# Performance work log

Measured on AMD Instinct MI355X. Metric: run time of the kernel, lower is better.

Reference implementation:

```python
import jax, jax.numpy as jnp
import numpy as np

D_MODEL, NHEAD, INT_DIM = 1024, 16, 4096
HEAD_DIM = D_MODEL // NHEAD
EPS = 1e-5


def _layernorm(x, gamma, beta):
    mu = jnp.mean(x, axis=-1, keepdims=True)
    var = jnp.var(x, axis=-1, keepdims=True)
    return (x - mu) * jax.lax.rsqrt(var + EPS) * gamma + beta


def setup_inputs() -> dict:
    key = jax.random.key(0)
    ks = jax.random.split(key, 16)
    B, T = 2, 2048
    s = 0.02
    inp = {
        'x': jax.random.normal(ks[0], (B, T, D_MODEL), dtype=jnp.float32),
        'Wq': jax.random.normal(ks[1], (D_MODEL, D_MODEL), dtype=jnp.float32) * s,
        'bq': jnp.zeros((D_MODEL,), jnp.float32),
        'Wk': jax.random.normal(ks[2], (D_MODEL, D_MODEL), dtype=jnp.float32) * s,
        'bk': jnp.zeros((D_MODEL,), jnp.float32),
        'Wv': jax.random.normal(ks[3], (D_MODEL, D_MODEL), dtype=jnp.float32) * s,
        'bv': jnp.zeros((D_MODEL,), jnp.float32),
        'Wo': jax.random.normal(ks[4], (D_MODEL, D_MODEL), dtype=jnp.float32) * s,
        'bo': jnp.zeros((D_MODEL,), jnp.float32),
        'ln1_g': jnp.ones((D_MODEL,), jnp.float32),
        'ln1_b': jnp.zeros((D_MODEL,), jnp.float32),
        'ln2_g': jnp.ones((D_MODEL,), jnp.float32),
        'ln2_b': jnp.zeros((D_MODEL,), jnp.float32),
        'W1': jax.random.normal(ks[5], (D_MODEL, INT_DIM), dtype=jnp.float32) * s,
        'b1': jnp.zeros((INT_DIM,), jnp.float32),
        'W2': jax.random.normal(ks[6], (INT_DIM, D_MODEL), dtype=jnp.float32) * s,
        'b2': jnp.zeros((D_MODEL,), jnp.float32),
    }
    return inp


def reference(x, Wq, bq, Wk, bk, Wv, bv, Wo, bo, ln1_g, ln1_b, ln2_g, ln2_b, W1, b1, W2, b2):
    B, T, D = x.shape
    # projections
    q = (x @ Wq + bq).reshape(B, T, NHEAD, HEAD_DIM).transpose(0, 2, 1, 3)
    k = (x @ Wk + bk).reshape(B, T, NHEAD, HEAD_DIM).transpose(0, 2, 1, 3)
    v = (x @ Wv + bv).reshape(B, T, NHEAD, HEAD_DIM).transpose(0, 2, 1, 3)
    # attention: [B,H,T,T] scores, softmax over keys
    scores = jnp.einsum('bhqd,bhkd->bhqk', q, k) / jnp.sqrt(jnp.float32(HEAD_DIM))
    attn = jax.nn.softmax(scores, axis=-1)
    out = jnp.einsum('bhqk,bhkd->bhqd', attn, v)
    out = out.transpose(0, 2, 1, 3).reshape(B, T, D)
    attn_output = out @ Wo + bo
    # residual + layernorm 1
    h = _layernorm(x + attn_output, ln1_g, ln1_b)
    # FFN
    ff = jax.nn.relu(h @ W1 + b1) @ W2 + b2
    # residual + layernorm 2
    return _layernorm(h + ff, ln2_g, ln2_b)
```

## Files before the change

kernel.cpp:

```cpp
#include <hip/hip_runtime.h>
#include <cstdint>

#define DEVI __device__ __forceinline__

typedef float f32x4 __attribute__((ext_vector_type(4)));
typedef __bf16 bf16x8 __attribute__((ext_vector_type(8)));
typedef unsigned int u32x4v __attribute__((ext_vector_type(4)));
typedef unsigned short u16;
typedef unsigned int u32;
typedef unsigned long long u64;

#define LOG2E 1.44269504088896f
#define QSCALE (0.125f * LOG2E)

DEVI u16 bf16bits(float f) {
    u32 u = __builtin_bit_cast(u32, f);
    u32 r = u + 0x7fffu + ((u >> 16) & 1u);
    return (u16)(r >> 16);
}

DEVI u32 pack2bf(float a, float b) {
    u16 x = __builtin_bit_cast(u16, (__bf16)a);
    u16 y = __builtin_bit_cast(u16, (__bf16)b);
    return (u32)x | ((u32)y << 16);
}

DEVI void gload16(const void* g, const void* l) {
    __builtin_amdgcn_global_load_lds(
        (const __attribute__((address_space(1))) void*)(u64)(uintptr_t)g,
        (__attribute__((address_space(3))) void*)(u32)(uintptr_t)l,
        16, 0, 0);
}

__global__ __launch_bounds__(256) void cast_bf16_kernel(const float* __restrict__ in,
                                                        u16* __restrict__ out, int n4) {
    int i = blockIdx.x * 256 + threadIdx.x;
    if (i < n4) {
        float4 v = ((const float4*)in)[i];
        u32 lo = bf16bits(v.x) | ((u32)bf16bits(v.y) << 16);
        u32 hi = bf16bits(v.z) | ((u32)bf16bits(v.w) << 16);
        ((uint2*)out)[i] = make_uint2(lo, hi);
    }
}

DEVI void tpose_body(const float* __restrict__ src, u16* __restrict__ dst, int K_, int N_) {
    __shared__ float t[64][65];
    int k0 = blockIdx.x * 64, n0 = blockIdx.y * 64;
    int tid = threadIdx.x;
#pragma unroll
    for (int i = 0; i < 16; i++) {
        int idx = i * 256 + tid;
        int r = idx >> 6, c = idx & 63;
        t[r][c] = src[(u64)(k0 + r) * N_ + n0 + c];
    }
    __syncthreads();
#pragma unroll
    for (int i = 0; i < 16; i++) {
        int idx = i * 256 + tid;
        int r = idx >> 6, c = idx & 63;
        dst[(u64)(n0 + r) * K_ + k0 + c] = bf16bits(t[c][r]);
    }
}

__global__ __launch_bounds__(256) void transpose_cast_kernel(const float* __restrict__ src,
                                                             u16* __restrict__ dst,
                                                             int K_, int N_) {
    tpose_body(src, dst, K_, N_);
}

__global__ __launch_bounds__(256) void transpose_cast4_kernel(
    const float* __restrict__ s0, const float* __restrict__ s1,
    const float* __restrict__ s2, const float* __restrict__ s3,
    u16* __restrict__ d0, u16* __restrict__ d1, u16* __restrict__ d2, u16* __restrict__ d3) {
    int z = blockIdx.z;
    const float* src = z == 0 ? s0 : z == 1 ? s1 : z == 2 ? s2 : s3;
    u16* dst = z == 0 ? d0 : z == 1 ? d1 : z == 2 ? d2 : d3;
    tpose_body(src, dst, 1024, 1024);
}

enum { MODE_QK = 0, MODE_VT = 1, MODE_RESID = 2, MODE_RELU = 3 };

DEVI void gemm_core(const u16* __restrict__ A, const u16* __restrict__ Bt, int K_,
                    u16* ldsA, u16* ldsB, f32x4 (&acc)[4][4], int m0, int n0) {
    const int tid = threadIdx.x;
    const int lane = tid & 63;
    const int wid = tid >> 6;
    const int wr = wid >> 1, wc = wid & 1;
    const int l15 = lane & 15, l4 = lane >> 4;

    for (int kt = 0; kt < K_; kt += 64) {
        __syncthreads();
#pragma unroll
        for (int i = 0; i < 4; i++) {
            int s = i * 256 + tid;
            int row = s >> 3, c = s & 7;
            gload16(A + (u64)(m0 + row) * K_ + kt + ((c ^ (row & 7)) * 8),
                    (const char*)ldsA + s * 16);
        }
#pragma unroll
        for (int i = 0; i < 4; i++) {
            int s = i * 256 + tid;
            int row = s >> 3, c = s & 7;
            gload16(Bt + (u64)(n0 + row) * K_ + kt + ((c ^ (row & 7)) * 8),
                    (const char*)ldsB + s * 16);
        }
        __syncthreads();
#pragma unroll
        for (int ks = 0; ks < 2; ks++) {
            bf16x8 af[4], bfr[4];
#pragma unroll
            for (int mi = 0; mi < 4; mi++) {
                int row = wr * 64 + mi * 16 + l15;
                af[mi] = *(const bf16x8*)((const char*)ldsA + row * 128 +
                                          (((ks * 4 + l4) ^ (row & 7)) * 16));
            }
#pragma unroll
            for (int ni = 0; ni < 4; ni++) {
                int row = wc * 64 + ni * 16 + l15;
                bfr[ni] = *(const bf16x8*)((const char*)ldsB + row * 128 +
                                           (((ks * 4 + l4) ^ (row & 7)) * 16));
            }
            __builtin_amdgcn_s_setprio(1);
#pragma unroll
            for (int mi = 0; mi < 4; mi++)
#pragma unroll
                for (int ni = 0; ni < 4; ni++)
                    acc[mi][ni] = __builtin_amdgcn_mfma_f32_16x16x32_bf16(
                        af[mi], bfr[ni], acc[mi][ni], 0, 0, 0);
            __builtin_amdgcn_s_setprio(0);
        }
    }
}

template <int MODE>
DEVI void gemm_epilogue(f32x4 (&acc)[4][4], const float* __restrict__ bias,
                        const float* __restrict__ resid, void* __restrict__ outp,
                        int N_, int m0, int n0, float scale) {
    const int tid = threadIdx.x;
    const int lane = tid & 63;
    const int wid = tid >> 6;
    const int wr = wid >> 1, wc = wid & 1;
    const int l15 = lane & 15, l4 = lane >> 4;
#pragma unroll
    for (int mi = 0; mi < 4; mi++) {
#pragma unroll
        for (int ni = 0; ni < 4; ni++) {
            const int n = n0 + wc * 64 + ni * 16 + l15;
            const float bv = bias[n];
            const int mb = m0 + wr * 64 + mi * 16 + l4 * 4;
            if (MODE == MODE_VT) {
                const int b = mb >> 11, t = mb & 2047;
                const int hh = n >> 6, d = n & 63;
                u32 lo = pack2bf(acc[mi][ni][0] + bv, acc[mi][ni][1] + bv);
                u32 hi = pack2bf(acc[mi][ni][2] + bv, acc[mi][ni][3] + bv);
                u64 idx = ((u64)((b << 4) + hh) * 64 + d) * 2048 + t;
                *(uint2*)((u16*)outp + idx) = make_uint2(lo, hi);
            } else {
#pragma unroll
                for (int r = 0; r < 4; r++) {
                    const int m = mb + r;
                    const float v = acc[mi][ni][r] + bv;
                    if (MODE == MODE_QK) {
                        const int b = m >> 11, t = m & 2047;
                        const int hh = n >> 6, d = n & 63;
                        ((u16*)outp)[(((u64)((b << 4) + hh) * 2048 + t) << 6) + d] =
                            bf16bits(v * scale);
                    } else if (MODE == MODE_RESID) {
                        const u64 i2 = (u64)m * N_ + n;
                        ((float*)outp)[i2] = v + resid[i2];
                    } else {
                        ((u16*)outp)[(u64)m * N_ + n] = bf16bits(fmaxf(v, 0.f));
                    }
                }
            }
        }
    }
}

template <int MODE>
__global__ __launch_bounds__(256, 2)
void gemm_kernel(const u16* __restrict__ A, const u16* __restrict__ Bt,
                 const float* __restrict__ bias, const float* __restrict__ resid,
                 void* __restrict__ outp, int N_, int K_) {
    __shared__ u16 ldsA[128 * 64];
    __shared__ u16 ldsB[128 * 64];
    const int m0 = blockIdx.x * 128;
    const int n0 = blockIdx.y * 128;
    f32x4 acc[4][4];
#pragma unroll
    for (int i = 0; i < 4; i++)
#pragma unroll
        for (int j = 0; j < 4; j++) acc[i][j] = (f32x4){0.f, 0.f, 0.f, 0.f};
    gemm_core(A, Bt, K_, ldsA, ldsB, acc, m0, n0);
    gemm_epilogue<MODE>(acc, bias, resid, outp, N_, m0, n0, 1.f);
}

__global__ __launch_bounds__(256, 2)
void gemm_qkv_kernel(const u16* __restrict__ A,
                     const u16* __restrict__ Wq, const u16* __restrict__ Wk,
                     const u16* __restrict__ Wv,
                     const float* __restrict__ bq, const float* __restrict__ bk,
                     const float* __restrict__ bv,
                     u16* __restrict__ Qo, u16* __restrict__ Ko, u16* __restrict__ Vo) {
    __shared__ u16 ldsA[128 * 64];
    __shared__ u16 ldsB[128 * 64];
    const int z = blockIdx.z;
    const u16* Bt = z == 0 ? Wq : z == 1 ? Wk : Wv;
    const float* bias = z == 0 ? bq : z == 1 ? bk : bv;
    const int m0 = blockIdx.x * 128;
    const int n0 = blockIdx.y * 128;
    f32x4 acc[4][4];
#pragma unroll
    for (int i = 0; i < 4; i++)
#pragma unroll
        for (int j = 0; j < 4; j++) acc[i][j] = (f32x4){0.f, 0.f, 0.f, 0.f};
    gemm_core(A, Bt, 1024, ldsA, ldsB, acc, m0, n0);
    if (z == 2)
        gemm_epilogue<MODE_VT>(acc, bias, nullptr, Vo, 1024, m0, n0, 1.f);
    else
        gemm_epilogue<MODE_QK>(acc, bias, nullptr, z == 0 ? Qo : Ko, 1024, m0, n0,
                               z == 0 ? QSCALE : 1.f);
}

__global__ __launch_bounds__(256, 5)
void attn_kernel(const u16* __restrict__ Qg, const u16* __restrict__ Kg,
                 const u16* __restrict__ Vtg, u16* __restrict__ Og) {
    __shared__ u16 ldsK[2][64 * 64];
    __shared__ u16 ldsV[2][64 * 64];
    const int tid = threadIdx.x;
    const int lane = tid & 63;
    const int w = tid >> 6;
    const int l15 = lane & 15, l4 = lane >> 4;
    const int id = blockIdx.x;
    const int swz = (id & 7) * 128 + (id >> 3);
    const int bh = swz >> 5;
    const int qblk = swz & 31;
    const u64 kvbase = (u64)bh * 2048 * 64;
    const int qw0 = qblk * 64 + w * 16;

    auto stage = [&](int buf, int kt) {
#pragma unroll
        for (int i = 0; i < 2; i++) {
            int s = i * 256 + tid; int row = s >> 3, c = s & 7;
            gload16(Kg + kvbase + (u64)(kt + row) * 64 + ((c ^ (row & 7)) * 8),
                    (const char*)ldsK[buf] + s * 16);
        }
#pragma unroll
        for (int i = 0; i < 2; i++) {
            int s = i * 256 + tid; int row = s >> 3, c = s & 7;
            gload16(Vtg + kvbase + (u64)row * 2048 + kt + ((c ^ (row & 7)) * 8),
                    (const char*)ldsV[buf] + s * 16);
        }
    };

    stage(0, 0);

    bf16x8 aq[2];
#pragma unroll
    for (int ks = 0; ks < 2; ks++)
        aq[ks] = *(const bf16x8*)(Qg + kvbase + (u64)(qw0 + l15) * 64 + ks * 32 + l4 * 8);

    f32x4 acco[4];
#pragma unroll
    for (int i = 0; i < 4; i++) acco[i] = (f32x4){0.f, 0.f, 0.f, 0.f};
    float la0 = 0.f, la1 = 0.f;

    asm volatile("s_waitcnt vmcnt(0)" ::: "memory");
    __builtin_amdgcn_s_barrier();

    for (int t = 0; t < 32; t++) {
        const int cur = t & 1;
        if (t < 31) stage(cur ^ 1, (t + 1) * 64);
        const u16* K_ = ldsK[cur];
        const u16* V_ = ldsV[cur];

        f32x4 sf[4];
#pragma unroll
        for (int f = 0; f < 4; f++) sf[f] = (f32x4){0.f, 0.f, 0.f, 0.f};
#pragma unroll
        for (int ks = 0; ks < 2; ks++) {
            bf16x8 ak[4];
#pragma unroll
            for (int f = 0; f < 4; f++) {
                int row = f * 16 + l15;
                ak[f] = *(const bf16x8*)((const char*)K_ + row * 128 +
                                         (((ks * 4 + l4) ^ (row & 7)) * 16));
            }
            __builtin_amdgcn_s_setprio(1);
#pragma unroll
            for (int f = 0; f < 4; f++)
                sf[f] = __builtin_amdgcn_mfma_f32_16x16x32_bf16(ak[f], aq[ks], sf[f], 0, 0, 0);
            __builtin_amdgcn_s_setprio(0);
        }

        u32 A[4], B[4];
#pragma unroll
        for (int f = 0; f < 4; f++) {
            float p0 = exp2f(sf[f][0]);
            float p1 = exp2f(sf[f][1]);
            float p2 = exp2f(sf[f][2]);
            float p3 = exp2f(sf[f][3]);
            la0 += p0 + p2;
            la1 += p1 + p3;
            A[f] = pack2bf(p0, p1);
            B[f] = pack2bf(p2, p3);
        }
        asm volatile("v_permlane32_swap_b32 %0, %1" : "+v"(A[0]), "+v"(A[1]));
        asm volatile("v_permlane16_swap_b32 %0, %1" : "+v"(A[0]), "+v"(A[1]));
        asm volatile("v_permlane32_swap_b32 %0, %1" : "+v"(B[0]), "+v"(B[1]));
        asm volatile("v_permlane16_swap_b32 %0, %1" : "+v"(B[0]), "+v"(B[1]));
        asm volatile("v_permlane32_swap_b32 %0, %1" : "+v"(A[2]), "+v"(A[3]));
        asm volatile("v_permlane16_swap_b32 %0, %1" : "+v"(A[2]), "+v"(A[3]));
        asm volatile("v_permlane32_swap_b32 %0, %1" : "+v"(B[2]), "+v"(B[3]));
        asm volatile("v_permlane16_swap_b32 %0, %1" : "+v"(B[2]), "+v"(B[3]));

#pragma unroll
        for (int ks = 0; ks < 2; ks++) {
            u32x4v pw = {A[2 * ks], B[2 * ks], A[2 * ks + 1], B[2 * ks + 1]};
            bf16x8 pfrag = __builtin_bit_cast(bf16x8, pw);
            bf16x8 av[4];
#pragma unroll
            for (int nf = 0; nf < 4; nf++) {
                int row = nf * 16 + l15;
                av[nf] = *(const bf16x8*)((const char*)V_ + row * 128 +
                                          (((ks * 4 + l4) ^ (row & 7)) * 16));
            }
            __builtin_amdgcn_s_setprio(1);
#pragma unroll
            for (int nf = 0; nf < 4; nf++)
                acco[nf] = __builtin_amdgcn_mfma_f32_16x16x32_bf16(av[nf], pfrag, acco[nf], 0, 0, 0);
            __builtin_amdgcn_s_setprio(0);
        }

        asm volatile("s_waitcnt vmcnt(0)" ::: "memory");
        __builtin_amdgcn_s_barrier();
    }

    float lacc = la0 + la1;
    lacc += __shfl_xor(lacc, 16, 64);
    lacc += __shfl_xor(lacc, 32, 64);
    const float inv = 1.f / lacc;

    const int b = bh >> 4, h = bh & 15;
    const int tq = qw0 + l15;
#pragma unroll
    for (int nf = 0; nf < 4; nf++) {
        const int d = nf * 16 + l4 * 4;
        u32 lo = pack2bf(acco[nf][0] * inv, acco[nf][1] * inv);
        u32 hi = pack2bf(acco[nf][2] * inv, acco[nf][3] * inv);
        *(uint2*)(Og + ((u64)(b * 2048 + tq) << 10) + h * 64 + d) = make_uint2(lo, hi);
    }
}

template <bool WB16>
__global__ __launch_bounds__(256, 4)
void ln_kernel(const float* __restrict__ in, const float* __restrict__ gam,
               const float* __restrict__ bet, float* __restrict__ outf,
               u16* __restrict__ outb) {
    __shared__ float red[2][4];
    const int row = blockIdx.x;
    const int tid = threadIdx.x;
    float4 v = ((const float4*)(in + (u64)row * 1024))[tid];
    float s = v.x + v.y + v.z + v.w;
    float sq = v.x * v.x + v.y * v.y + v.z * v.z + v.w * v.w;
#pragma unroll
    for (int sh = 1; sh < 64; sh <<= 1) {
        s += __shfl_xor(s, sh, 64);
        sq += __shfl_xor(sq, sh, 64);
    }
    if ((tid & 63) == 0) { red[0][tid >> 6] = s; red[1][tid >> 6] = sq; }
    __syncthreads();
    s = red[0][0] + red[0][1] + red[0][2] + red[0][3];
    sq = red[1][0] + red[1][1] + red[1][2] + red[1][3];
    float mu = s * (1.f / 1024.f);
    float var = sq * (1.f / 1024.f) - mu * mu;
    float inv = rsqrtf(var + 1e-5f);
    float4 g = ((const float4*)gam)[tid];
    float4 bb = ((const float4*)bet)[tid];
    float4 o;
    o.x = (v.x - mu) * inv * g.x + bb.x;
    o.y = (v.y - mu) * inv * g.y + bb.y;
    o.z = (v.z - mu) * inv * g.z + bb.z;
    o.w = (v.w - mu) * inv * g.w + bb.w;
    ((float4*)(outf + (u64)row * 1024))[tid] = o;
    if (WB16) {
        u32 lo = pack2bf(o.x, o.y);
        u32 hi = pack2bf(o.z, o.w);
        ((uint2*)(outb + (u64)row * 1024))[tid] = make_uint2(lo, hi);
    }
}

extern "C" void kernel_launch(void* const* d_in, const int* in_sizes, int n_in,
                              void* d_out, int out_size, void* d_ws, size_t ws_size,
                              hipStream_t stream) {
    (void)in_sizes; (void)n_in; (void)out_size; (void)ws_size;
    const float* x  = (const float*)d_in[0];
    const float* Wq = (const float*)d_in[1];
    const float* bq = (const float*)d_in[2];
    const float* Wk = (const float*)d_in[3];
    const float* bk = (const float*)d_in[4];
    const float* Wv = (const float*)d_in[5];
    const float* bv = (const float*)d_in[6];
    const float* Wo = (const float*)d_in[7];
    const float* bo = (const float*)d_in[8];
    const float* g1 = (const float*)d_in[9];
    const float* be1 = (const float*)d_in[10];
    const float* g2 = (const float*)d_in[11];
    const float* be2 = (const float*)d_in[12];
    const float* W1 = (const float*)d_in[13];
    const float* b1 = (const float*)d_in[14];
    const float* W2 = (const float*)d_in[15];
    const float* b2 = (const float*)d_in[16];

    char* ws = (char*)d_ws;
    const u64 MB = 1024ull * 1024ull;
    u16* xb    = (u16*)(ws + 0);
    u16* Wqt   = (u16*)(ws + 8 * MB);
    u16* Wkt   = (u16*)(ws + 10 * MB);
    u16* Wvt   = (u16*)(ws + 12 * MB);
    u16* Wot   = (u16*)(ws + 14 * MB);
    u16* W1t   = (u16*)(ws + 16 * MB);
    u16* W2t   = (u16*)(ws + 24 * MB);
    u16* Qb    = (u16*)(ws + 32 * MB);
    u16* Kb    = (u16*)(ws + 40 * MB);
    u16* Vtb   = (u16*)(ws + 48 * MB);
    u16* Ob    = (u16*)(ws + 56 * MB);
    float* pre1 = (float*)(ws + 64 * MB);
    float* hf  = (float*)(ws + 80 * MB);
    u16* hb    = (u16*)(ws + 96 * MB);
    u16* ffb   = (u16*)(ws + 104 * MB);
    float* pre2 = (float*)(ws + 64 * MB);

    cast_bf16_kernel<<<4096, 256, 0, stream>>>(x, xb, 1024 * 1024);
    transpose_cast4_kernel<<<dim3(16, 16, 4), 256, 0, stream>>>(Wq, Wk, Wv, Wo,
                                                                Wqt, Wkt, Wvt, Wot);
    transpose_cast_kernel<<<dim3(16, 64), 256, 0, stream>>>(W1, W1t, 1024, 4096);
    transpose_cast_kernel<<<dim3(64, 16), 256, 0, stream>>>(W2, W2t, 4096, 1024);

    gemm_qkv_kernel<<<dim3(32, 8, 3), 256, 0, stream>>>(xb, Wqt, Wkt, Wvt,
                                                        bq, bk, bv, Qb, Kb, Vtb);

    attn_kernel<<<1024, 256, 0, stream>>>(Qb, Kb, Vtb, Ob);

    gemm_kernel<MODE_RESID><<<dim3(32, 8), 256, 0, stream>>>(Ob, Wot, bo, x, pre1, 1024, 1024);
    ln_kernel<true><<<4096, 256, 0, stream>>>(pre1, g1, be1, hf, hb);
    gemm_kernel<MODE_RELU><<<dim3(32, 32), 256, 0, stream>>>(hb, W1t, b1, nullptr, ffb, 4096, 1024);
    gemm_kernel<MODE_RESID><<<dim3(32, 8), 256, 0, stream>>>(ffb, W2t, b2, hf, pre2, 1024, 4096);
    ln_kernel<false><<<4096, 256, 0, stream>>>(pre2, g2, be2, (float*)d_out, nullptr);
}
```

Before: 248.5 us.

## Merge prep kernels and use 128x64 double-buffered GEMM for N=1024 outputs

Folds the x cast and all four weight transpose-cast launches into one prep kernel, which removes three launches. Adds a new GEMM kernel with 128x64 tiles, double-buffered LDS and async global-to-LDS loads, used for the Wo and W2 projections. The smaller tile doubles the block count for these N=1024 GEMMs (256 to 512 blocks), which should fill the CUs better. The cost is more redundant A-tile loads and a different epilogue store pattern.

```diff
diff --git a/kernel.cpp b/kernel.cpp
--- a/kernel.cpp
+++ b/kernel.cpp
@@ -32,21 +32,45 @@
         16, 0, 0);
 }
 
-__global__ __launch_bounds__(256) void cast_bf16_kernel(const float* __restrict__ in,
-                                                        u16* __restrict__ out, int n4) {
-    int i = blockIdx.x * 256 + threadIdx.x;
-    if (i < n4) {
-        float4 v = ((const float4*)in)[i];
-        u32 lo = bf16bits(v.x) | ((u32)bf16bits(v.y) << 16);
-        u32 hi = bf16bits(v.z) | ((u32)bf16bits(v.w) << 16);
-        ((uint2*)out)[i] = make_uint2(lo, hi);
-    }
-}
-
-DEVI void tpose_body(const float* __restrict__ src, u16* __restrict__ dst, int K_, int N_) {
+__global__ __launch_bounds__(256)
+void prep_kernel(const float* __restrict__ x, u16* __restrict__ xb,
+                 const float* __restrict__ Wq, const float* __restrict__ Wk,
+                 const float* __restrict__ Wv, const float* __restrict__ Wo,
+                 u16* __restrict__ Wqt, u16* __restrict__ Wkt,
+                 u16* __restrict__ Wvt, u16* __restrict__ Wot,
+                 const float* __restrict__ W1, u16* __restrict__ W1t,
+                 const float* __restrict__ W2, u16* __restrict__ W2t) {
     __shared__ float t[64][65];
-    int k0 = blockIdx.x * 64, n0 = blockIdx.y * 64;
-    int tid = threadIdx.x;
+    const int b = blockIdx.x;
+    const int tid = threadIdx.x;
+    if (b < 4096) {
+        int i = b * 256 + tid;
+        float4 v = ((const float4*)x)[i];
+        u32 lo = pack2bf(v.x, v.y);
+        u32 hi = pack2bf(v.z, v.w);
+        ((uint2*)xb)[i] = make_uint2(lo, hi);
+        return;
+    }
+    const float* src;
+    u16* dst;
+    int K_, N_, k0, n0;
+    if (b < 5120) {
+        int l = b - 4096;
+        int z = l >> 8;
+        l &= 255;
+        src = z == 0 ? Wq : z == 1 ? Wk : z == 2 ? Wv : Wo;
+        dst = z == 0 ? Wqt : z == 1 ? Wkt : z == 2 ? Wvt : Wot;
+        K_ = 1024; N_ = 1024;
+        k0 = (l & 15) * 64; n0 = (l >> 4) * 64;
+    } else if (b < 6144) {
+        int l = b - 5120;
+        src = W1; dst = W1t; K_ = 1024; N_ = 4096;
+        k0 = (l & 15) * 64; n0 = (l >> 4) * 64;
+    } else {
+        int l = b - 6144;
+        src = W2; dst = W2t; K_ = 4096; N_ = 1024;
+        k0 = (l & 63) * 64; n0 = (l >> 6) * 64;
+    }
 #pragma unroll
     for (int i = 0; i < 16; i++) {
         int idx = i * 256 + tid;
@@ -60,22 +84,6 @@
         int r = idx >> 6, c = idx & 63;
         dst[(u64)(n0 + r) * K_ + k0 + c] = bf16bits(t[c][r]);
     }
-}
-
-__global__ __launch_bounds__(256) void transpose_cast_kernel(const float* __restrict__ src,
-                                                             u16* __restrict__ dst,
-                                                             int K_, int N_) {
-    tpose_body(src, dst, K_, N_);
-}
-
-__global__ __launch_bounds__(256) void transpose_cast4_kernel(
-    const float* __restrict__ s0, const float* __restrict__ s1,
-    const float* __restrict__ s2, const float* __restrict__ s3,
-    u16* __restrict__ d0, u16* __restrict__ d1, u16* __restrict__ d2, u16* __restrict__ d3) {
-    int z = blockIdx.z;
-    const float* src = z == 0 ? s0 : z == 1 ? s1 : z == 2 ? s2 : s3;
-    u16* dst = z == 0 ? d0 : z == 1 ? d1 : z == 2 ? d2 : d3;
-    tpose_body(src, dst, 1024, 1024);
 }
 
 enum { MODE_QK = 0, MODE_VT = 1, MODE_RESID = 2, MODE_RELU = 3 };
@@ -220,6 +228,94 @@
     else
         gemm_epilogue<MODE_QK>(acc, bias, nullptr, z == 0 ? Qo : Ko, 1024, m0, n0,
                                z == 0 ? QSCALE : 1.f);
+}
+
+__global__ __launch_bounds__(256, 2)
+void gemm_n64_kernel(const u16* __restrict__ A, const u16* __restrict__ Bt,
+                     const float* __restrict__ bias, const float* __restrict__ resid,
+                     float* __restrict__ outp, int K_) {
+    __shared__ u16 ldsA[2][128 * 64];
+    __shared__ u16 ldsB[2][64 * 64];
+    const int tid = threadIdx.x;
+    const int lane = tid & 63;
+    const int wid = tid >> 6;
+    const int m0 = blockIdx.x * 128;
+    const int n0 = blockIdx.y * 64;
+    const int l15 = lane & 15, l4 = lane >> 4;
+
+    auto stage = [&](int buf, int kt) {
+#pragma unroll
+        for (int i = 0; i < 4; i++) {
+            int s = i * 256 + tid;
+            int row = s >> 3, c = s & 7;
+            gload16(A + (u64)(m0 + row) * K_ + kt + ((c ^ (row & 7)) * 8),
+                    (const char*)ldsA[buf] + s * 16);
+        }
+#pragma unroll
+        for (int i = 0; i < 2; i++) {
+            int s = i * 256 + tid;
+            int row = s >> 3, c = s & 7;
+            gload16(Bt + (u64)(n0 + row) * K_ + kt + ((c ^ (row & 7)) * 8),
+                    (const char*)ldsB[buf] + s * 16);
+        }
+    };
+
+    f32x4 acc[2][4];
+#pragma unroll
+    for (int i = 0; i < 2; i++)
+#pragma unroll
+        for (int j = 0; j < 4; j++) acc[i][j] = (f32x4){0.f, 0.f, 0.f, 0.f};
+
+    stage(0, 0);
+    const int nk = K_ >> 6;
+    for (int t = 0; t < nk; t++) {
+        const int cur = t & 1;
+        asm volatile("s_waitcnt vmcnt(0)" ::: "memory");
+        __builtin_amdgcn_s_barrier();
+        if (t + 1 < nk) stage(cur ^ 1, (t + 1) * 64);
+        const u16* A_ = ldsA[cur];
+        const u16* B_ = ldsB[cur];
+#pragma unroll
+        for (int ks = 0; ks < 2; ks++) {
+            bf16x8 af[2], bfr[4];
+#pragma unroll
+            for (int mi = 0; mi < 2; mi++) {
+                int row = wid * 32 + mi * 16 + l15;
+                af[mi] = *(const bf16x8*)((const char*)A_ + row * 128 +
+                                          (((ks * 4 + l4) ^ (row & 7)) * 16));
+            }
+#pragma unroll
+            for (int ni = 0; ni < 4; ni++) {
+                int row = ni * 16 + l15;
+                bfr[ni] = *(const bf16x8*)((const char*)B_ + row * 128 +
+                                           (((ks * 4 + l4) ^ (row & 7)) * 16));
+            }
+            __builtin_amdgcn_s_setprio(1);
+#pragma unroll
+            for (int mi = 0; mi < 2; mi++)
+#pragma unroll
+                for (int ni = 0; ni < 4; ni++)
+                    acc[mi][ni] = __builtin_amdgcn_mfma_f32_16x16x32_bf16(
+                        af[mi], bfr[ni], acc[mi][ni], 0, 0, 0);
+            __builtin_amdgcn_s_setprio(0);
+        }
+        __builtin_amdgcn_s_barrier();
+    }
+
+#pragma unroll
+    for (int mi = 0; mi < 2; mi++) {
+#pragma unroll
+        for (int ni = 0; ni < 4; ni++) {
+            const int n = n0 + ni * 16 + l15;
+            const float bv = bias[n];
+            const int mb = m0 + wid * 32 + mi * 16 + l4 * 4;
+#pragma unroll
+            for (int r = 0; r < 4; r++) {
+                const u64 i2 = (u64)(mb + r) * 1024 + n;
+                outp[i2] = acc[mi][ni][r] + bv + resid[i2];
+            }
+        }
+    }
 }
 
 __global__ __launch_bounds__(256, 5)
@@ -431,20 +527,17 @@
     u16* ffb   = (u16*)(ws + 104 * MB);
     float* pre2 = (float*)(ws + 64 * MB);
 
-    cast_bf16_kernel<<<4096, 256, 0, stream>>>(x, xb, 1024 * 1024);
-    transpose_cast4_kernel<<<dim3(16, 16, 4), 256, 0, stream>>>(Wq, Wk, Wv, Wo,
-                                                                Wqt, Wkt, Wvt, Wot);
-    transpose_cast_kernel<<<dim3(16, 64), 256, 0, stream>>>(W1, W1t, 1024, 4096);
-    transpose_cast_kernel<<<dim3(64, 16), 256, 0, stream>>>(W2, W2t, 4096, 1024);
+    prep_kernel<<<7168, 256, 0, stream>>>(x, xb, Wq, Wk, Wv, Wo,
+                                          Wqt, Wkt, Wvt, Wot, W1, W1t, W2, W2t);
 
     gemm_qkv_kernel<<<dim3(32, 8, 3), 256, 0, stream>>>(xb, Wqt, Wkt, Wvt,
                                                         bq, bk, bv, Qb, Kb, Vtb);
 
     attn_kernel<<<1024, 256, 0, stream>>>(Qb, Kb, Vtb, Ob);
 
-    gemm_kernel<MODE_RESID><<<dim3(32, 8), 256, 0, stream>>>(Ob, Wot, bo, x, pre1, 1024, 1024);
+    gemm_n64_kernel<<<dim3(32, 16), 256, 0, stream>>>(Ob, Wot, bo, x, pre1, 1024);
     ln_kernel<true><<<4096, 256, 0, stream>>>(pre1, g1, be1, hf, hb);
     gemm_kernel<MODE_RELU><<<dim3(32, 32), 256, 0, stream>>>(hb, W1t, b1, nullptr, ffb, 4096, 1024);
-    gemm_kernel<MODE_RESID><<<dim3(32, 8), 256, 0, stream>>>(ffb, W2t, b2, hf, pre2, 1024, 4096);
+    gemm_n64_kernel<<<dim3(32, 16), 256, 0, stream>>>(ffb, W2t, b2, hf, pre2, 4096);
     ln_kernel<false><<<4096, 256, 0, stream>>>(pre2, g2, be2, (float*)d_out, nullptr);
 }
```

After: 214.5 us. 13.7% less time.
